# Kernel optimization log

Measured on AMD Instinct MI355X. Metric: run time of the kernel, lower is better.

The kernel has to match this reference:

```python
import jax, jax.numpy as jnp
import numpy as np

B = 1024        # batch of query guides
D = 768         # d_model
M = 50000       # memory bank size
K = 50          # k_neighbors
H = 8           # attention heads
HD = D // H     # head dim = 96
GH = 256        # gate hidden


def setup_inputs() -> dict:
    key = jax.random.key(0)
    ks = jax.random.split(key, 16)
    s = 0.02
    return {
        "query": jax.random.normal(ks[0], (B, D), jnp.float32),
        # memory bank buffers (initialized via initialize_memory in the original)
        "memory_keys": jax.random.normal(ks[1], (M, D), jnp.float32),
        "memory_values": jax.random.uniform(ks[2], (M, 1), jnp.float32, 0.5, 1.0),
        # MultiheadAttention in/out projections (batch_first, embed_dim=D, 8 heads)
        "Wq": jax.random.normal(ks[3], (D, D), jnp.float32) * s,
        "bq": jnp.zeros((D,), jnp.float32),
        "Wk": jax.random.normal(ks[4], (D, D), jnp.float32) * s,
        "bk": jnp.zeros((D,), jnp.float32),
        "Wv": jax.random.normal(ks[5], (D, D), jnp.float32) * s,
        "bv": jnp.zeros((D,), jnp.float32),
        "Wo": jax.random.normal(ks[6], (D, D), jnp.float32) * s,
        "bo": jnp.zeros((D,), jnp.float32),
        # gate MLP: Linear(2D, 256) -> ReLU -> Linear(256, 1) -> Sigmoid
        "Wg1": jax.random.normal(ks[7], (GH, 2 * D), jnp.float32) * s,
        "bg1": jnp.zeros((GH,), jnp.float32),
        "Wg2": jax.random.normal(ks[8], (1, GH), jnp.float32) * s,
        "bg2": jnp.zeros((1,), jnp.float32),
    }


def reference(query, memory_keys, memory_values,
              Wq, bq, Wk, bk, Wv, bv, Wo, bo, Wg1, bg1, Wg2, bg2):
    b = query.shape[0]
    # ---- retrieval: euclidean cdist + smallest-k ----
    q2 = jnp.sum(query * query, axis=-1, keepdims=True)      # (B,1)
    m2 = jnp.sum(memory_keys * memory_keys, axis=-1)          # (M,)
    d2 = q2 + m2[None, :] - 2.0 * (query @ memory_keys.T)     # (B,M)
    dists = jnp.sqrt(jnp.maximum(d2, 0.0))
    neg_top, idx = jax.lax.top_k(-dists, K)                   # smallest K
    distances = -neg_top                                      # (B,K)
    neighbor_keys = memory_keys[idx]                          # (B,K,D)
    neighbor_vals = memory_values[idx]                        # (B,K,1)

    # ---- cross-attention: 1 query token attending to K neighbors ----
    q = (query @ Wq.T + bq).reshape(b, H, HD)                 # (B,H,HD)
    kp = (neighbor_keys @ Wk.T + bk).reshape(b, K, H, HD)     # (B,K,H,HD)
    vp = (neighbor_keys @ Wv.T + bv).reshape(b, K, H, HD)
    scores = jnp.einsum('bhd,bkhd->bhk', q, kp) / jnp.sqrt(jnp.float32(HD))
    attn = jax.nn.softmax(scores, axis=-1)                    # (B,H,K)
    ctx = jnp.einsum('bhk,bkhd->bhd', attn, vp).reshape(b, D)
    context = ctx @ Wo.T + bo                                 # (B,D)

    similarity = jnp.exp(-distances / jnp.mean(distances))    # scalar mean over all
    weights = similarity / jnp.sum(similarity, axis=1, keepdims=True)
    rag_prediction = jnp.sum(neighbor_vals * weights[..., None], axis=1)  # (B,1)

    # ---- gated fusion ----
    combined = jnp.concatenate([query, context], axis=-1)     # (B,2D)
    hgate = jax.nn.relu(combined @ Wg1.T + bg1)
    gate_weight = jax.nn.sigmoid(hgate @ Wg2.T + bg2)         # (B,1)

    enhanced_embeddings = query + context                     # (B,D)
    return enhanced_embeddings, rag_prediction, gate_weight
```

## Files before the change

### kernel.cpp

```cpp
#include <hip/hip_runtime.h>

typedef unsigned int u32;
typedef unsigned short u16;
typedef unsigned char u8;
typedef signed char s8;
typedef unsigned long long u64;
typedef __bf16 bf16x8 __attribute__((ext_vector_type(8)));
typedef float f32x4 __attribute__((ext_vector_type(4)));
typedef int i32x4 __attribute__((ext_vector_type(4)));

#define DEVI __device__ __forceinline__

DEVI u16 f2bf(float x){ u32 u = __builtin_bit_cast(u32, x); return (u16)((u + 0x7fffu + ((u>>16)&1u)) >> 16); }
DEVI float bf2f(u16 h){ return __builtin_bit_cast(float, ((u32)h)<<16); }
DEVI u32 qz(float x){ int i = (int)rintf(x*25.4f); i = i>127?127:(i<-127?-127:i); return (u32)(u8)(s8)i; }

#define NB 1024
#define ND 768
#define NM 50000
#define NK 50
#define NH 8
#define CAP 2048
#define CAPX 256
#define S22 0.0031000062f
#define QINV 0.0393700787f

__global__ __launch_bounds__(256) void prep_all(const float* __restrict__ query, const float* __restrict__ mkeys,
    const float* __restrict__ Wq, const float* __restrict__ Wv, const float* __restrict__ Wo,
    const float* __restrict__ Wg1, const float* __restrict__ Wk,
    u16* __restrict__ qb, float* __restrict__ q2, s8* __restrict__ qi8, float* __restrict__ thr,
    s8* __restrict__ mi8, float* __restrict__ m2,
    u16* __restrict__ wqb, u16* __restrict__ wvb, u16* __restrict__ wob,
    u16* __restrict__ wg1b, u16* __restrict__ wkt)
{
  const int bid = blockIdx.x, t = threadIdx.x;
  if (bid < 12500){
    int r = bid*4 + (t>>6);
    int l = t & 63;
    const float4* s4 = (const float4*)(mkeys + (long)r*ND);
    u32* di = (u32*)(mi8 + (long)r*ND);
    float ss = 0.f;
    #pragma unroll
    for (int j=0;j<3;j++){
      float4 v = s4[l + j*64];
      ss += v.x*v.x + v.y*v.y + v.z*v.z + v.w*v.w;
      di[l+j*64] = qz(v.x) | (qz(v.y)<<8) | (qz(v.z)<<16) | (qz(v.w)<<24);
    }
    #pragma unroll
    for (int o=32;o;o>>=1) ss += __shfl_down(ss,o);
    if (l==0) m2[r]=ss;
  } else if (bid < 12756){
    int r = (bid-12500)*4 + (t>>6);
    int l = t & 63;
    const float4* s4 = (const float4*)(query + (long)r*ND);
    u32* dq = (u32*)(qb + (long)r*ND);
    u32* di = (u32*)(qi8 + (long)r*ND);
    float ss = 0.f;
    #pragma unroll
    for (int j=0;j<3;j++){
      float4 v = s4[l + j*64];
      ss += v.x*v.x + v.y*v.y + v.z*v.z + v.w*v.w;
      dq[(l+j*64)*2]   = ((u32)f2bf(v.y)<<16) | f2bf(v.x);
      dq[(l+j*64)*2+1] = ((u32)f2bf(v.w)<<16) | f2bf(v.z);
      di[l+j*64] = qz(v.x) | (qz(v.y)<<8) | (qz(v.z)<<16) | (qz(v.w)<<24);
    }
    #pragma unroll
    for (int o=32;o;o>>=1) ss += __shfl_down(ss,o);
    if (l==0){
      q2[r]=ss;
      thr[r] = ss + (float)ND - 2.5f*sqrtf(2.f*(float)ND + 4.f*ss);
    }
  } else {
    long i = (long)(bid-12756)*256 + t;
    const long NW = (long)ND*ND;
    if (i < NW){ wqb[i] = f2bf(Wq[i]); return; }
    i -= NW;
    if (i < NW){ wvb[i] = f2bf(Wv[i]); return; }
    i -= NW;
    if (i < NW){ wob[i] = f2bf(Wo[i]); return; }
    i -= NW;
    if (i < 256*2*ND){ wg1b[i] = f2bf(Wg1[i]); return; }
    i -= 256*2*ND;
    int h = (int)(i / (ND*96)); int rem = (int)(i % (ND*96)); int d = rem / 96; int hd = rem % 96;
    wkt[i] = f2bf(Wk[(long)(h*96+hd)*ND + d]);
  }
}

DEVI void i8_tile(u8* __restrict__ As, u8* __restrict__ Bs,
                  int m0, int n0, int cxcd,
                  const s8* __restrict__ A, int lda,
                  const s8* __restrict__ Bm, int ldb,
                  int Ndim, int Kbytes,
                  const float* __restrict__ q2, const float* __restrict__ m2, const float* __restrict__ thr,
                  float* __restrict__ cand_d2, int* __restrict__ cand_idx, int* __restrict__ cnt)
{
  const int t = threadIdx.x;
  const int lane = t & 63, w = t >> 6;
  i32x4 acc[2][8];
  #pragma unroll
  for (int m=0;m<2;m++)
    #pragma unroll
    for (int n=0;n<8;n++) acc[m][n] = i32x4{0,0,0,0};

  const int ra = t>>1, c0 = (t&1)*2;
  const int rb1 = ra+64;
  const int sw = (ra>>1)&3;
  const int s0 = ((c0  )^sw)*16, s1 = ((c0+1)^sw)*16;
  int jb0 = n0+ra;  if (jb0>=Ndim) jb0=Ndim-1;
  int jb1 = n0+rb1; if (jb1>=Ndim) jb1=Ndim-1;
  const s8* pa  = &A[(long)(m0+ra)*lda + c0*16];
  const s8* pb0 = &Bm[(long)jb0*ldb + c0*16];
  const s8* pb1 = &Bm[(long)jb1*ldb + c0*16];

  for (int k0=0; k0<Kbytes; k0+=64){
    __syncthreads();
    uint4 a0  = *(const uint4*)(pa  + k0);
    uint4 a1  = *(const uint4*)(pa  + k0 + 16);
    uint4 b00 = *(const uint4*)(pb0 + k0);
    uint4 b01 = *(const uint4*)(pb0 + k0 + 16);
    uint4 b10 = *(const uint4*)(pb1 + k0);
    uint4 b11 = *(const uint4*)(pb1 + k0 + 16);
    *(uint4*)&As[ra*64 + s0]  = a0;
    *(uint4*)&As[ra*64 + s1]  = a1;
    *(uint4*)&Bs[ra*64 + s0]  = b00;
    *(uint4*)&Bs[ra*64 + s1]  = b01;
    *(uint4*)&Bs[rb1*64 + s0] = b10;
    *(uint4*)&Bs[rb1*64 + s1] = b11;
    __syncthreads();
    i32x4 af[2], bfr[8];
    #pragma unroll
    for (int m=0;m<2;m++){
      int row = w*32 + m*16 + (lane&15);
      int slot = ((lane>>4) ^ ((row>>1)&3));
      af[m] = __builtin_bit_cast(i32x4, *(const uint4*)&As[row*64 + slot*16]);
    }
    #pragma unroll
    for (int n=0;n<8;n++){
      int row = n*16 + (lane&15);
      int slot = ((lane>>4) ^ ((row>>1)&3));
      bfr[n] = __builtin_bit_cast(i32x4, *(const uint4*)&Bs[row*64 + slot*16]);
    }
    #pragma unroll
    for (int m=0;m<2;m++)
      #pragma unroll
      for (int n=0;n<8;n++)
        acc[m][n] = __builtin_amdgcn_mfma_i32_16x16x64_i8(af[m], bfr[n], acc[m][n], 0,0,0);
  }

  const int g = lane>>4, li = lane&15;
  #pragma unroll
  for (int m=0;m<2;m++){
    #pragma unroll
    for (int q=0;q<4;q++){
      int r = m0 + w*32 + m*16 + (g<<2) + q;
      float qv = q2[r];
      float tv = thr[r];
      #pragma unroll
      for (int n=0;n<8;n++){
        int c = n0 + n*16 + li;
        int cc = c < Ndim ? c : 0;
        float v = S22 * (float)acc[m][n][q];
        float d2 = fmaxf(qv+m2[cc]-v, 0.f);
        bool hit = (c<Ndim) && (d2 <= tv);
        u64 mask = __ballot(hit);
        u32 bits = (u32)((mask >> (g*16)) & 0xffffull);
        int base = 0;
        if (li==0 && bits) base = atomicAdd(&cnt[cxcd*NB + r], (int)__popc(bits));
        base = __shfl(base, g*16);
        if (hit){
          int slot = base + (int)__popc(bits & ((1u<<li)-1u));
          if (slot < CAPX){
            cand_d2[(long)r*CAP + cxcd*CAPX + slot] = d2;
            cand_idx[(long)r*CAP + cxcd*CAPX + slot] = c;
          }
        }
      }
    }
  }
}

template<int FOUT>
DEVI void bf_tile(u16* __restrict__ As, u16* __restrict__ Bs,
                  int m0, int n0, int z,
                  const u16* __restrict__ A, int lda, long az,
                  const u16* __restrict__ Bm, int ldb, long bz,
                  int Ndim, int Kdim,
                  u16* __restrict__ Cb, float* __restrict__ Cf, int ldc, long cz,
                  const float* __restrict__ bias)
{
  A += (long)z*az; Bm += (long)z*bz;
  const int t = threadIdx.x;
  const int lane = t & 63, w = t >> 6;
  f32x4 acc[2][8];
  #pragma unroll
  for (int m=0;m<2;m++)
    #pragma unroll
    for (int n=0;n<8;n++) acc[m][n] = f32x4{0.f,0.f,0.f,0.f};

  const int ra = t>>1, c0 = (t&1)*2;
  const int rb1 = ra+64;
  const int sw = (ra>>1)&3;
  const int s0 = ((c0  )^sw)*8, s1 = ((c0+1)^sw)*8;
  int jb0 = n0+ra;  if (jb0>=Ndim) jb0=Ndim-1;
  int jb1 = n0+rb1; if (jb1>=Ndim) jb1=Ndim-1;
  const u16* pa  = &A[(long)(m0+ra)*lda + c0*8];
  const u16* pb0 = &Bm[(long)jb0*ldb + c0*8];
  const u16* pb1 = &Bm[(long)jb1*ldb + c0*8];

  for (int k0=0; k0<Kdim; k0+=32){
    __syncthreads();
    uint4 a0  = *(const uint4*)(pa  + k0);
    uint4 a1  = *(const uint4*)(pa  + k0 + 8);
    uint4 b00 = *(const uint4*)(pb0 + k0);
    uint4 b01 = *(const uint4*)(pb0 + k0 + 8);
    uint4 b10 = *(const uint4*)(pb1 + k0);
    uint4 b11 = *(const uint4*)(pb1 + k0 + 8);
    *(uint4*)&As[ra*32 + s0]  = a0;
    *(uint4*)&As[ra*32 + s1]  = a1;
    *(uint4*)&Bs[ra*32 + s0]  = b00;
    *(uint4*)&Bs[ra*32 + s1]  = b01;
    *(uint4*)&Bs[rb1*32 + s0] = b10;
    *(uint4*)&Bs[rb1*32 + s1] = b11;
    __syncthreads();
    bf16x8 af[2], bfr[8];
    #pragma unroll
    for (int m=0;m<2;m++){
      int row = w*32 + m*16 + (lane&15);
      int slot = ((lane>>4) ^ ((row>>1)&3));
      af[m] = __builtin_bit_cast(bf16x8, *(const uint4*)&As[row*32 + slot*8]);
    }
    #pragma unroll
    for (int n=0;n<8;n++){
      int row = n*16 + (lane&15);
      int slot = ((lane>>4) ^ ((row>>1)&3));
      bfr[n] = __builtin_bit_cast(bf16x8, *(const uint4*)&Bs[row*32 + slot*8]);
    }
    #pragma unroll
    for (int m=0;m<2;m++)
      #pragma unroll
      for (int n=0;n<8;n++)
        acc[m][n] = __builtin_amdgcn_mfma_f32_16x16x32_bf16(af[m], bfr[n], acc[m][n], 0,0,0);
  }

  #pragma unroll
  for (int m=0;m<2;m++){
    #pragma unroll
    for (int q=0;q<4;q++){
      int r = m0 + w*32 + m*16 + ((lane>>4)<<2) + q;
      #pragma unroll
      for (int n=0;n<8;n++){
        int c = n0 + n*16 + (lane&15);
        if (c >= Ndim) continue;
        float v = acc[m][n][q];
        if (bias) v += bias[c];
        if (FOUT==0) Cb[(long)r*ldc + (long)z*cz + c] = f2bf(v);
        else         Cf[(long)r*ldc + c] = v;
      }
    }
  }
}

__global__ __launch_bounds__(128)
void mega_a(const u16* __restrict__ qb, const u16* __restrict__ wqb,
            u16* __restrict__ qpb, const float* __restrict__ bq,
            const u16* __restrict__ wg1b, float* __restrict__ hg, const float* __restrict__ bg1)
{
  __shared__ u8 smem[12288];
  const int bid = blockIdx.x;
  if (bid < 96){
    int bx = bid & 15, by = bid >> 4;
    bf_tile<0>((u16*)smem, (u16*)(smem+4096), bx*64, by*128, 0,
               qb, ND, 0, wqb, ND, 0, ND, ND, qpb, nullptr, ND, 0, bq);
  } else {
    int b2 = bid - 96;
    int bx = b2 & 15, by = b2 >> 4;
    bf_tile<1>((u16*)smem, (u16*)(smem+4096), bx*64, by*128, 0,
               qb, ND, 0, wg1b, 2*ND, 0, 256, ND, nullptr, hg, 256, 0, bg1);
  }
}

__global__ __launch_bounds__(128)
void mega_b(const s8* __restrict__ qi8, const s8* __restrict__ mi8,
            const float* __restrict__ q2, const float* __restrict__ m2, const float* __restrict__ thr,
            float* __restrict__ cand_d2, int* __restrict__ cand_idx, int* __restrict__ cnt,
            const u16* __restrict__ qpb, const u16* __restrict__ wkt, u16* __restrict__ ubuf)
{
  __shared__ u8 smem[12288];
  const int bid = blockIdx.x;
  if (bid < 6272){
    int cxcd = bid & 7, j = bid >> 3;
    int xt = j & 15, yhi = j >> 4;
    int y = yhi*8 + cxcd;
    if (y >= 391) return;
    i8_tile(smem, smem+4096, xt*64, y*128, cxcd, qi8, ND, mi8, ND, NM, ND,
            q2, m2, thr, cand_d2, cand_idx, cnt);
  } else {
    int b2 = bid - 6272;
    int bx = b2 & 15, r = b2 >> 4;
    int by = r % 6, z = r / 6;
    bf_tile<0>((u16*)smem, (u16*)(smem+4096), bx*64, by*128, z,
               qpb, ND, 96, wkt, 96, (long)ND*96, ND, 96, ubuf, nullptr, NH*ND, ND, nullptr);
  }
}

template<int MODE>
__global__ __launch_bounds__(256)
void gemm_uni(const u16* __restrict__ A, int lda, long az,
              const u16* __restrict__ Bm, int ldb, long bz,
              int Ndim, int Kdim,
              float* __restrict__ Cf, u16* __restrict__ Cb, int ldc, long cz,
              const float* __restrict__ bias, long biasz,
              const float* __restrict__ qsrc, u16* __restrict__ out2, int ldo2)
{
  const int m0 = blockIdx.x*128, n0 = blockIdx.y*128, z = blockIdx.z;
  A += (long)z*az; Bm += (long)z*bz;

  const int t = threadIdx.x;
  const int lane = t & 63, wid = t >> 6;
  __shared__ u16 As[2][128*32], Bs[2][128*32];
  f32x4 acc[4][4];
  #pragma unroll
  for (int m=0;m<4;m++)
    #pragma unroll
    for (int n=0;n<4;n++) acc[m][n] = f32x4{0.f,0.f,0.f,0.f};

  const int wr = (wid>>1)*64, wc = (wid&1)*64;
  const int sr = t>>2, sc4 = t&3;
  const int r0 = sr, r1 = sr+64;
  const int sl0 = (sc4 ^ ((r0>>1)&3))*8, sl1 = (sc4 ^ ((r1>>1)&3))*8;
  int jb0 = n0+r0; if (jb0>=Ndim) jb0=Ndim-1;
  int jb1 = n0+r1; if (jb1>=Ndim) jb1=Ndim-1;
  const u16* pa0 = &A[(long)(m0+r0)*lda + sc4*8];
  const u16* pa1 = &A[(long)(m0+r1)*lda + sc4*8];
  const u16* pb0 = &Bm[(long)jb0*ldb + sc4*8];
  const u16* pb1 = &Bm[(long)jb1*ldb + sc4*8];

  uint4 pA0,pA1,pB0,pB1, qA0,qA1,qB0,qB1;
  #define LOADG(S, K0) { S##A0 = *(const uint4*)(pa0+(K0)); S##A1 = *(const uint4*)(pa1+(K0)); \
                         S##B0 = *(const uint4*)(pb0+(K0)); S##B1 = *(const uint4*)(pb1+(K0)); }
  #define STORELDS(BUF, S) { *(uint4*)&As[BUF][r0*32+sl0] = S##A0; *(uint4*)&As[BUF][r1*32+sl1] = S##A1; \
                             *(uint4*)&Bs[BUF][r0*32+sl0] = S##B0; *(uint4*)&Bs[BUF][r1*32+sl1] = S##B1; }

  auto compute = [&](const u16* __restrict__ Ab, const u16* __restrict__ Bb){
    bf16x8 af[4], bfr[4];
    #pragma unroll
    for (int m=0;m<4;m++){
      int row = wr + m*16 + (lane&15);
      int slot = ((lane>>4) ^ ((row>>1)&3));
      af[m] = __builtin_bit_cast(bf16x8, *(const uint4*)&Ab[row*32 + slot*8]);
    }
    #pragma unroll
    for (int n=0;n<4;n++){
      int row = wc + n*16 + (lane&15);
      int slot = ((lane>>4) ^ ((row>>1)&3));
      bfr[n] = __builtin_bit_cast(bf16x8, *(const uint4*)&Bb[row*32 + slot*8]);
    }
    #pragma unroll
    for (int m=0;m<4;m++)
      #pragma unroll
      for (int n=0;n<4;n++)
        acc[m][n] = __builtin_amdgcn_mfma_f32_16x16x32_bf16(af[m], bfr[n], acc[m][n], 0,0,0);
  };

  const int nt = Kdim >> 5;
  LOADG(p, 0);
  if (nt > 1) LOADG(q, 32);
  #pragma unroll 1
  for (int ti=0; ti<nt; ti+=2){
    STORELDS(0, p);
    asm volatile("s_waitcnt lgkmcnt(0)" ::: "memory");
    __builtin_amdgcn_s_barrier();
    if (ti+2 < nt) LOADG(p, (ti+2)*32);
    compute(As[0], Bs[0]);
    if (ti+1 < nt){
      STORELDS(1, q);
      asm volatile("s_waitcnt lgkmcnt(0)" ::: "memory");
      __builtin_amdgcn_s_barrier();
      if (ti+3 < nt) LOADG(q, (ti+3)*32);
      compute(As[1], Bs[1]);
    }
  }
  #undef LOADG
  #undef STORELDS

  const float* bz_p = bias ? bias + (long)z*biasz : nullptr;
  #pragma unroll
  for (int m=0;m<4;m++){
    #pragma unroll
    for (int n=0;n<4;n++){
      #pragma unroll
      for (int q=0;q<4;q++){
        int r = m0 + wr + m*16 + ((lane>>4)<<2) + q;
        int c = n0 + wc + n*16 + (lane&15);
        float v = acc[m][n][q];
        if (MODE==1){
          if (c<Ndim){ if(bz_p) v += bz_p[c]; Cb[(long)r*ldc + (long)z*cz + c] = f2bf(v); }
        } else if (MODE==5){
          if (c<Ndim){ Cf[(long)r*ldc + c] = fmaxf(Cf[(long)r*ldc + c] + v, 0.f); }
        } else {
          if (c<Ndim){
            float ctx = v + (bz_p?bz_p[c]:0.f);
            out2[(long)r*ldo2 + c] = f2bf(ctx);
            Cf[(long)r*ldc + c] = qsrc[(long)r*ND+c] + ctx;
          }
        }
      }
    }
  }
}

__global__ __launch_bounds__(256) void selattn(
    const float* __restrict__ cand_d2, const int* __restrict__ cand_idx, const int* __restrict__ cnt,
    const s8* __restrict__ mi8, const u16* __restrict__ ub,
    int* __restrict__ sel, float* __restrict__ dists, float* __restrict__ dsum,
    u16* __restrict__ sb)
{
  const int b = blockIdx.x, t = threadIdx.x;
  __shared__ u8 smemA[25*772*2];
  u64* arr = (u64*)smemA;
  u16* nkS = (u16*)smemA;
  __shared__ u16 uS[8*772];
  __shared__ float sc[NH*32];
  __shared__ float mh[NH], dh[NH], scS[NH];
  __shared__ int selS[NK];
  __shared__ float dS[NK];
  __shared__ int cS[8], oS[9];

  {
    const u32* src = (const u32*)&ub[(long)b*NH*ND];
    for (int i=t;i<NH*(ND/2);i+=256){
      int h = i/(ND/2), d = i%(ND/2);
      ((u32*)&uS[h*772])[d] = src[h*(ND/2)+d];
    }
  }
  if (t < 8){ int c = cnt[t*NB + b]; cS[t] = c > CAPX ? CAPX : c; }
  if (t >= 64 && t < 64+NH){ mh[t-64] = -1e30f; dh[t-64] = 0.f; }
  __syncthreads();
  if (t == 0){ oS[0]=0; for (int s=0;s<8;s++) oS[s+1]=oS[s]+cS[s]; }
  if (t < NK){ dS[t]=0.f; selS[t]=0; }
  __syncthreads();
  const int n = oS[8];
  for (int i=t;i<8*CAPX;i+=256){
    int s = i>>8, pos = i&(CAPX-1);
    if (pos < cS[s]){
      float d2 = fmaxf(cand_d2[(long)b*CAP + s*CAPX + pos],0.f);
      arr[oS[s]+pos] = ((u64)__builtin_bit_cast(u32, d2)<<32) | (u32)cand_idx[(long)b*CAP + s*CAPX + pos];
    }
  }
  __syncthreads();
  for (int i=t;i<n;i+=256){
    u64 me = arr[i];
    int rank = 0;
    for (int j=0;j<n;j++) rank += (arr[j] < me) ? 1 : 0;
    if (rank < NK){
      selS[rank] = (int)(u32)(me & 0xffffffffu);
      dS[rank] = sqrtf(__builtin_bit_cast(float, (u32)(me>>32)));
    }
  }
  __syncthreads();
  if (t < NK){ sel[b*NK+t] = selS[t]; dists[b*NK+t] = dS[t]; }
  if (t==0){ float s=0.f; for (int r=0;r<NK;r++) s+=dS[r]; dsum[b]=s; }
  __syncthreads();

  float sacc[3][NH];
  #pragma unroll
  for (int j=0;j<3;j++)
    #pragma unroll
    for (int h=0;h<NH;h++) sacc[j][h]=0.f;
  const float rs = 0.10206207261596575f;

  for (int half=0; half<2; ++half){
    if (half) __syncthreads();
    for (int k=0;k<25;k++){
      const u32* src = (const u32*)&mi8[(long)selS[half*25+k]*ND];
      if (t < 192){
        u32 a = src[t];
        float f0 = (float)(s8)(a & 0xff);
        float f1 = (float)(s8)((a>>8) & 0xff);
        float f2 = (float)(s8)((a>>16) & 0xff);
        float f3 = (float)(s8)(a>>24);
        u64 pk = (u64)f2bf(f0*QINV) | ((u64)f2bf(f1*QINV)<<16)
               | ((u64)f2bf(f2*QINV)<<32) | ((u64)f2bf(f3*QINV)<<48);
        *(u64*)&nkS[k*772 + t*4] = pk;
      }
    }
    __syncthreads();
    if (t < 200){
      const u32* nr = (const u32*)&nkS[(t%25)*772];
      const u32* ur = (const u32*)&uS[(t/25)*772];
      float acc = 0.f;
      #pragma unroll 8
      for (int d=0; d<ND/2; d++){
        u32 a = nr[d], uu = ur[d];
        acc += bf2f((u16)a)*bf2f((u16)uu) + bf2f((u16)(a>>16))*bf2f((u16)(uu>>16));
      }
      sc[(t/25)*32 + (t%25)] = acc*rs;
    }
    __syncthreads();
    if (t < NH){
      float mn = mh[t];
      #pragma unroll
      for (int k=0;k<25;k++) mn = fmaxf(mn, sc[t*32+k]);
      float scale = __expf(mh[t]-mn);
      float d = dh[t]*scale;
      #pragma unroll
      for (int k=0;k<25;k++){ float e = __expf(sc[t*32+k]-mn); sc[t*32+k]=e; d+=e; }
      mh[t]=mn; dh[t]=d; scS[t]=scale;
    }
    __syncthreads();
    #pragma unroll
    for (int j=0;j<3;j++){
      int dd = t + j*256;
      #pragma unroll
      for (int h=0;h<NH;h++) sacc[j][h] *= scS[h];
      for (int k=0;k<25;k++){
        float nv = bf2f(nkS[k*772+dd]);
        float w0,w1,w2,w3,w4,w5,w6,w7;
        w0=sc[0*32+k]; w1=sc[1*32+k]; w2=sc[2*32+k]; w3=sc[3*32+k];
        w4=sc[4*32+k]; w5=sc[5*32+k]; w6=sc[6*32+k]; w7=sc[7*32+k];
        sacc[j][0]+=w0*nv; sacc[j][1]+=w1*nv; sacc[j][2]+=w2*nv; sacc[j][3]+=w3*nv;
        sacc[j][4]+=w4*nv; sacc[j][5]+=w5*nv; sacc[j][6]+=w6*nv; sacc[j][7]+=w7*nv;
      }
    }
  }
  float inv[NH];
  #pragma unroll
  for (int h=0;h<NH;h++) inv[h] = 1.f/dh[h];
  #pragma unroll
  for (int j=0;j<3;j++){
    int dd = t + j*256;
    #pragma unroll
    for (int h=0;h<NH;h++) sb[(long)b*NH*ND + h*ND + dd] = f2bf(sacc[j][h]*inv[h]);
  }
}

__global__ void mean_kernel(const float* __restrict__ dsum, float* __restrict__ meanbuf){
  int t = threadIdx.x;
  float s=0.f; for (int i=t;i<NB;i+=256) s += dsum[i];
  __shared__ float red[256];
  red[t]=s; __syncthreads();
  #pragma unroll
  for (int st=128;st>0;st>>=1){ if(t<st) red[t]+=red[t+st]; __syncthreads(); }
  if (t==0){ float mean = red[0]/(float)(NB*NK); meanbuf[0]=mean; meanbuf[1]=1.f/mean; }
}

__global__ void final_k(const float* __restrict__ hg, const float* __restrict__ Wg2,
                        const float* __restrict__ bg2,
                        const int* __restrict__ sel, const float* __restrict__ dists,
                        const float* __restrict__ mvals, const float* __restrict__ meanbuf,
                        float* __restrict__ out_rag, float* __restrict__ out_gate){
  int b = blockIdx.x*4 + (threadIdx.x>>6);
  int l = threadIdx.x & 63;
  float s=0.f;
  for (int i=l;i<256;i+=64) s += hg[(long)b*256+i]*Wg2[i];
  float num=0.f, den=0.f;
  if (l < NK){
    float d = dists[b*NK+l];
    float v = mvals[sel[b*NK+l]];
    float e = __expf(-d*meanbuf[1]);
    num = e*v; den = e;
  }
  #pragma unroll
  for (int o=32;o;o>>=1){ s += __shfl_down(s,o); num += __shfl_down(num,o); den += __shfl_down(den,o); }
  if (l==0){
    out_gate[b] = 1.f/(1.f+__expf(-(s+bg2[0])));
    out_rag[b]  = num/den;
  }
}

extern "C" void kernel_launch(void* const* d_in, const int* in_sizes, int n_in,
                              void* d_out, int out_size, void* d_ws, size_t ws_size,
                              hipStream_t stream){
  const float* query = (const float*)d_in[0];
  const float* mkeys = (const float*)d_in[1];
  const float* mvals = (const float*)d_in[2];
  const float* Wq  = (const float*)d_in[3];
  const float* bq  = (const float*)d_in[4];
  const float* Wk  = (const float*)d_in[5];
  const float* Wv  = (const float*)d_in[7];
  const float* bv  = (const float*)d_in[8];
  const float* Wo  = (const float*)d_in[9];
  const float* bo  = (const float*)d_in[10];
  const float* Wg1 = (const float*)d_in[11];
  const float* bg1 = (const float*)d_in[12];
  const float* Wg2 = (const float*)d_in[13];
  const float* bg2 = (const float*)d_in[14];
  float* out = (float*)d_out;

  char* ws = (char*)d_ws;
  size_t off = 0;
  auto alloc = [&](size_t bytes)->char*{ char* p = ws + off; off += (bytes + 255) & ~(size_t)255; return p; };

  s8*    mi8   = (s8*)   alloc((size_t)NM*ND);
  s8*    qi8   = (s8*)   alloc((size_t)NB*ND);
  u16*   qb    = (u16*)  alloc((size_t)NB*ND*2);
  float* q2    = (float*)alloc(NB*4);
  float* m2    = (float*)alloc(NM*4);
  u16*   wqb   = (u16*)  alloc((size_t)ND*ND*2);
  u16*   wkt   = (u16*)  alloc((size_t)ND*ND*2);
  u16*   wvb   = (u16*)  alloc((size_t)ND*ND*2);
  u16*   wob   = (u16*)  alloc((size_t)ND*ND*2);
  u16*   wg1b  = (u16*)  alloc((size_t)256*2*ND*2);
  float* cand_d2 = (float*)alloc((size_t)NB*CAP*4);
  int*   cand_idx= (int*)  alloc((size_t)NB*CAP*4);
  float* thr   = (float*)alloc(NB*4);
  int*   cnt   = (int*)  alloc(8*NB*4);
  int*   sel   = (int*)  alloc((size_t)NB*NK*4);
  float* dists = (float*)alloc((size_t)NB*NK*4);
  float* dsum  = (float*)alloc(NB*4);
  float* meanbuf=(float*)alloc(256);
  u16*   qpb   = (u16*)  alloc((size_t)NB*ND*2);
  u16*   ubuf  = (u16*)  alloc((size_t)NB*NH*ND*2);
  u16*   sbuf  = (u16*)  alloc((size_t)NB*NH*ND*2);
  u16*   ctx2b = (u16*)  alloc((size_t)NB*ND*2);
  u16*   ctxb  = (u16*)  alloc((size_t)NB*ND*2);
  float* hg    = (float*)alloc((size_t)NB*256*4);
  (void)ws_size; (void)in_sizes; (void)n_in; (void)out_size;

  prep_all<<<23508, 256, 0, stream>>>(query, mkeys, Wq, Wv, Wo, Wg1, Wk,
      qb, q2, qi8, thr, mi8, m2, wqb, wvb, wob, wg1b, wkt);
  hipMemsetAsync(cnt, 0, 8*NB*sizeof(int), stream);

  mega_a<<<128, 128, 0, stream>>>(qb, wqb, qpb, bq, wg1b, hg, bg1);

  mega_b<<<7040, 128, 0, stream>>>(qi8, mi8, q2, m2, thr, cand_d2, cand_idx, cnt,
      qpb, wkt, ubuf);

  selattn<<<NB, 256, 0, stream>>>(cand_d2, cand_idx, cnt, mi8, ubuf, sel, dists, dsum, sbuf);
  mean_kernel<<<1, 256, 0, stream>>>(dsum, meanbuf);

  gemm_uni<1><<<dim3(NB/128, 1, NH), 256, 0, stream>>>(sbuf,NH*ND,ND, wvb,ND,(long)96*ND, 96,ND,
      nullptr,ctx2b,ND,96, bv,96, nullptr,nullptr,0);

  gemm_uni<4><<<dim3(NB/128, ND/128, 1), 256, 0, stream>>>(ctx2b,ND,0, wob,ND,0, ND,ND,
      out,nullptr,ND,0, bo,0, query, ctxb, ND);

  gemm_uni<5><<<dim3(NB/128, 2, 1), 256, 0, stream>>>(ctxb,ND,0, wg1b+ND,2*ND,0, 256,ND,
      hg,nullptr,256,0, nullptr,0, nullptr,nullptr,0);

  final_k<<<NB/4, 256, 0, stream>>>(hg, Wg2, bg2, sel, dists, mvals, meanbuf,
      out + (size_t)NB*ND, out + (size_t)NB*ND + NB);
}
```

Before: 445.1 us.

## Fold counter reset into prep, move gate GEMM into mega_b, shrink tail GEMM tiles

Zeroing of the candidate counters moves out of a separate memset and into extra blocks of the prep kernel, which saves one launch. The query-half gate GEMM moves from mega_a into mega_b as extra blocks, so it runs alongside the retrieval tiles. The three tail GEMMs change from 128x128 tiles with 256 threads and a double-buffered pipeline to 64x128 tiles with 128 threads and a single buffer. This gives more blocks on these small problems, at the cost of losing the load/compute overlap.

```diff
diff --git a/kernel.cpp b/kernel.cpp
--- a/kernel.cpp
+++ b/kernel.cpp
@@ -31,7 +31,7 @@
     u16* __restrict__ qb, float* __restrict__ q2, s8* __restrict__ qi8, float* __restrict__ thr,
     s8* __restrict__ mi8, float* __restrict__ m2,
     u16* __restrict__ wqb, u16* __restrict__ wvb, u16* __restrict__ wob,
-    u16* __restrict__ wg1b, u16* __restrict__ wkt)
+    u16* __restrict__ wg1b, u16* __restrict__ wkt, int* __restrict__ cnt)
 {
   const int bid = blockIdx.x, t = threadIdx.x;
   if (bid < 12500){
@@ -70,7 +70,7 @@
       q2[r]=ss;
       thr[r] = ss + (float)ND - 2.5f*sqrtf(2.f*(float)ND + 4.f*ss);
     }
-  } else {
+  } else if (bid < 23508){
     long i = (long)(bid-12756)*256 + t;
     const long NW = (long)ND*ND;
     if (i < NW){ wqb[i] = f2bf(Wq[i]); return; }
@@ -83,6 +83,9 @@
     i -= 256*2*ND;
     int h = (int)(i / (ND*96)); int rem = (int)(i % (ND*96)); int d = rem / 96; int hd = rem % 96;
     wkt[i] = f2bf(Wk[(long)(h*96+hd)*ND + d]);
+  } else {
+    int i = (bid-23508)*256 + t;
+    cnt[i] = 0; cnt[i+2048] = 0; cnt[i+4096] = 0; cnt[i+6144] = 0;
   }
 }
 
@@ -262,28 +265,22 @@
 
 __global__ __launch_bounds__(128)
 void mega_a(const u16* __restrict__ qb, const u16* __restrict__ wqb,
-            u16* __restrict__ qpb, const float* __restrict__ bq,
-            const u16* __restrict__ wg1b, float* __restrict__ hg, const float* __restrict__ bg1)
+            u16* __restrict__ qpb, const float* __restrict__ bq)
 {
   __shared__ u8 smem[12288];
   const int bid = blockIdx.x;
-  if (bid < 96){
-    int bx = bid & 15, by = bid >> 4;
-    bf_tile<0>((u16*)smem, (u16*)(smem+4096), bx*64, by*128, 0,
-               qb, ND, 0, wqb, ND, 0, ND, ND, qpb, nullptr, ND, 0, bq);
-  } else {
-    int b2 = bid - 96;
-    int bx = b2 & 15, by = b2 >> 4;
-    bf_tile<1>((u16*)smem, (u16*)(smem+4096), bx*64, by*128, 0,
-               qb, ND, 0, wg1b, 2*ND, 0, 256, ND, nullptr, hg, 256, 0, bg1);
-  }
+  int bx = bid & 15, by = bid >> 4;
+  bf_tile<0>((u16*)smem, (u16*)(smem+4096), bx*64, by*128, 0,
+             qb, ND, 0, wqb, ND, 0, ND, ND, qpb, nullptr, ND, 0, bq);
 }
 
 __global__ __launch_bounds__(128)
 void mega_b(const s8* __restrict__ qi8, const s8* __restrict__ mi8,
             const float* __restrict__ q2, const float* __restrict__ m2, const float* __restrict__ thr,
             float* __restrict__ cand_d2, int* __restrict__ cand_idx, int* __restrict__ cnt,
-            const u16* __restrict__ qpb, const u16* __restrict__ wkt, u16* __restrict__ ubuf)
+            const u16* __restrict__ qpb, const u16* __restrict__ wkt, u16* __restrict__ ubuf,
+            const u16* __restrict__ qb, const u16* __restrict__ wg1b,
+            float* __restrict__ hg, const float* __restrict__ bg1)
 {
   __shared__ u8 smem[12288];
   const int bid = blockIdx.x;
@@ -294,115 +291,104 @@
     if (y >= 391) return;
     i8_tile(smem, smem+4096, xt*64, y*128, cxcd, qi8, ND, mi8, ND, NM, ND,
             q2, m2, thr, cand_d2, cand_idx, cnt);
-  } else {
+  } else if (bid < 7040){
     int b2 = bid - 6272;
     int bx = b2 & 15, r = b2 >> 4;
     int by = r % 6, z = r / 6;
     bf_tile<0>((u16*)smem, (u16*)(smem+4096), bx*64, by*128, z,
                qpb, ND, 96, wkt, 96, (long)ND*96, ND, 96, ubuf, nullptr, NH*ND, ND, nullptr);
+  } else {
+    int b2 = bid - 7040;
+    int bx = b2 & 15, by = b2 >> 4;
+    bf_tile<1>((u16*)smem, (u16*)(smem+4096), bx*64, by*128, 0,
+               qb, ND, 0, wg1b, 2*ND, 0, 256, ND, nullptr, hg, 256, 0, bg1);
   }
 }
 
 template<int MODE>
-__global__ __launch_bounds__(256)
-void gemm_uni(const u16* __restrict__ A, int lda, long az,
+__global__ __launch_bounds__(128)
+void gemm64_t(const u16* __restrict__ A, int lda, long az,
               const u16* __restrict__ Bm, int ldb, long bz,
               int Ndim, int Kdim,
               float* __restrict__ Cf, u16* __restrict__ Cb, int ldc, long cz,
-              const float* __restrict__ bias, long biasz,
+              const float* __restrict__ bias,
               const float* __restrict__ qsrc, u16* __restrict__ out2, int ldo2)
 {
-  const int m0 = blockIdx.x*128, n0 = blockIdx.y*128, z = blockIdx.z;
+  const int m0 = blockIdx.x*64, n0 = blockIdx.y*128, z = blockIdx.z;
   A += (long)z*az; Bm += (long)z*bz;
-
+  __shared__ u16 As[64*32], Bs[128*32];
   const int t = threadIdx.x;
-  const int lane = t & 63, wid = t >> 6;
-  __shared__ u16 As[2][128*32], Bs[2][128*32];
-  f32x4 acc[4][4];
-  #pragma unroll
-  for (int m=0;m<4;m++)
-    #pragma unroll
-    for (int n=0;n<4;n++) acc[m][n] = f32x4{0.f,0.f,0.f,0.f};
-
-  const int wr = (wid>>1)*64, wc = (wid&1)*64;
-  const int sr = t>>2, sc4 = t&3;
-  const int r0 = sr, r1 = sr+64;
-  const int sl0 = (sc4 ^ ((r0>>1)&3))*8, sl1 = (sc4 ^ ((r1>>1)&3))*8;
-  int jb0 = n0+r0; if (jb0>=Ndim) jb0=Ndim-1;
-  int jb1 = n0+r1; if (jb1>=Ndim) jb1=Ndim-1;
-  const u16* pa0 = &A[(long)(m0+r0)*lda + sc4*8];
-  const u16* pa1 = &A[(long)(m0+r1)*lda + sc4*8];
-  const u16* pb0 = &Bm[(long)jb0*ldb + sc4*8];
-  const u16* pb1 = &Bm[(long)jb1*ldb + sc4*8];
-
-  uint4 pA0,pA1,pB0,pB1, qA0,qA1,qB0,qB1;
-  #define LOADG(S, K0) { S##A0 = *(const uint4*)(pa0+(K0)); S##A1 = *(const uint4*)(pa1+(K0)); \
-                         S##B0 = *(const uint4*)(pb0+(K0)); S##B1 = *(const uint4*)(pb1+(K0)); }
-  #define STORELDS(BUF, S) { *(uint4*)&As[BUF][r0*32+sl0] = S##A0; *(uint4*)&As[BUF][r1*32+sl1] = S##A1; \
-                             *(uint4*)&Bs[BUF][r0*32+sl0] = S##B0; *(uint4*)&Bs[BUF][r1*32+sl1] = S##B1; }
-
-  auto compute = [&](const u16* __restrict__ Ab, const u16* __restrict__ Bb){
-    bf16x8 af[4], bfr[4];
-    #pragma unroll
-    for (int m=0;m<4;m++){
-      int row = wr + m*16 + (lane&15);
+  const int lane = t & 63, w = t >> 6;
+  f32x4 acc[2][8];
+  #pragma unroll
+  for (int m=0;m<2;m++)
+    #pragma unroll
+    for (int n=0;n<8;n++) acc[m][n] = f32x4{0.f,0.f,0.f,0.f};
+
+  const int ra = t>>1, c0 = (t&1)*2;
+  const int rb1 = ra+64;
+  const int sw = (ra>>1)&3;
+  const int s0 = ((c0  )^sw)*8, s1 = ((c0+1)^sw)*8;
+  int jb0 = n0+ra;  if (jb0>=Ndim) jb0=Ndim-1;
+  int jb1 = n0+rb1; if (jb1>=Ndim) jb1=Ndim-1;
+  const u16* pa  = &A[(long)(m0+ra)*lda + c0*8];
+  const u16* pb0 = &Bm[(long)jb0*ldb + c0*8];
+  const u16* pb1 = &Bm[(long)jb1*ldb + c0*8];
+
+  for (int k0=0; k0<Kdim; k0+=32){
+    __syncthreads();
+    uint4 a0  = *(const uint4*)(pa  + k0);
+    uint4 a1  = *(const uint4*)(pa  + k0 + 8);
+    uint4 b00 = *(const uint4*)(pb0 + k0);
+    uint4 b01 = *(const uint4*)(pb0 + k0 + 8);
+    uint4 b10 = *(const uint4*)(pb1 + k0);
+    uint4 b11 = *(const uint4*)(pb1 + k0 + 8);
+    *(uint4*)&As[ra*32 + s0]  = a0;
+    *(uint4*)&As[ra*32 + s1]  = a1;
+    *(uint4*)&Bs[ra*32 + s0]  = b00;
+    *(uint4*)&Bs[ra*32 + s1]  = b01;
+    *(uint4*)&Bs[rb1*32 + s0] = b10;
+    *(uint4*)&Bs[rb1*32 + s1] = b11;
+    __syncthreads();
+    bf16x8 af[2], bfr[8];
+    #pragma unroll
+    for (int m=0;m<2;m++){
+      int row = w*32 + m*16 + (lane&15);
       int slot = ((lane>>4) ^ ((row>>1)&3));
-      af[m] = __builtin_bit_cast(bf16x8, *(const uint4*)&Ab[row*32 + slot*8]);
-    }
-    #pragma unroll
-    for (int n=0;n<4;n++){
-      int row = wc + n*16 + (lane&15);
+      af[m] = __builtin_bit_cast(bf16x8, *(const uint4*)&As[row*32 + slot*8]);
+    }
+    #pragma unroll
+    for (int n=0;n<8;n++){
+      int row = n*16 + (lane&15);
       int slot = ((lane>>4) ^ ((row>>1)&3));
-      bfr[n] = __builtin_bit_cast(bf16x8, *(const uint4*)&Bb[row*32 + slot*8]);
-    }
-    #pragma unroll
-    for (int m=0;m<4;m++)
-      #pragma unroll
-      for (int n=0;n<4;n++)
+      bfr[n] = __builtin_bit_cast(bf16x8, *(const uint4*)&Bs[row*32 + slot*8]);
+    }
+    #pragma unroll
+    for (int m=0;m<2;m++)
+      #pragma unroll
+      for (int n=0;n<8;n++)
         acc[m][n] = __builtin_amdgcn_mfma_f32_16x16x32_bf16(af[m], bfr[n], acc[m][n], 0,0,0);
-  };
-
-  const int nt = Kdim >> 5;
-  LOADG(p, 0);
-  if (nt > 1) LOADG(q, 32);
-  #pragma unroll 1
-  for (int ti=0; ti<nt; ti+=2){
-    STORELDS(0, p);
-    asm volatile("s_waitcnt lgkmcnt(0)" ::: "memory");
-    __builtin_amdgcn_s_barrier();
-    if (ti+2 < nt) LOADG(p, (ti+2)*32);
-    compute(As[0], Bs[0]);
-    if (ti+1 < nt){
-      STORELDS(1, q);
-      asm volatile("s_waitcnt lgkmcnt(0)" ::: "memory");
-      __builtin_amdgcn_s_barrier();
-      if (ti+3 < nt) LOADG(q, (ti+3)*32);
-      compute(As[1], Bs[1]);
-    }
-  }
-  #undef LOADG
-  #undef STORELDS
-
-  const float* bz_p = bias ? bias + (long)z*biasz : nullptr;
-  #pragma unroll
-  for (int m=0;m<4;m++){
-    #pragma unroll
-    for (int n=0;n<4;n++){
-      #pragma unroll
-      for (int q=0;q<4;q++){
-        int r = m0 + wr + m*16 + ((lane>>4)<<2) + q;
-        int c = n0 + wc + n*16 + (lane&15);
+  }
+
+  #pragma unroll
+  for (int m=0;m<2;m++){
+    #pragma unroll
+    for (int q=0;q<4;q++){
+      int r = m0 + w*32 + m*16 + ((lane>>4)<<2) + q;
+      #pragma unroll
+      for (int n=0;n<8;n++){
+        int c = n0 + n*16 + (lane&15);
+        if (c >= Ndim) continue;
         float v = acc[m][n][q];
         if (MODE==1){
-          if (c<Ndim){ if(bz_p) v += bz_p[c]; Cb[(long)r*ldc + (long)z*cz + c] = f2bf(v); }
+          if (bias) v += bias[c];
+          Cb[(long)r*ldc + (long)z*cz + c] = f2bf(v);
         } else if (MODE==5){
-          if (c<Ndim){ Cf[(long)r*ldc + c] = fmaxf(Cf[(long)r*ldc + c] + v, 0.f); }
+          Cf[(long)r*ldc + c] = fmaxf(Cf[(long)r*ldc + c] + v, 0.f);
         } else {
-          if (c<Ndim){
-            float ctx = v + (bz_p?bz_p[c]:0.f);
-            out2[(long)r*ldo2 + c] = f2bf(ctx);
-            Cf[(long)r*ldc + c] = qsrc[(long)r*ND+c] + ctx;
-          }
+          float ctx = v + (bias?bias[c]:0.f);
+          out2[(long)r*ldo2 + c] = f2bf(ctx);
+          Cf[(long)r*ldc + c] = qsrc[(long)r*ND+c] + ctx;
         }
       }
     }
@@ -617,26 +603,25 @@
   float* hg    = (float*)alloc((size_t)NB*256*4);
   (void)ws_size; (void)in_sizes; (void)n_in; (void)out_size;
 
-  prep_all<<<23508, 256, 0, stream>>>(query, mkeys, Wq, Wv, Wo, Wg1, Wk,
-      qb, q2, qi8, thr, mi8, m2, wqb, wvb, wob, wg1b, wkt);
-  hipMemsetAsync(cnt, 0, 8*NB*sizeof(int), stream);
-
-  mega_a<<<128, 128, 0, stream>>>(qb, wqb, qpb, bq, wg1b, hg, bg1);
-
-  mega_b<<<7040, 128, 0, stream>>>(qi8, mi8, q2, m2, thr, cand_d2, cand_idx, cnt,
-      qpb, wkt, ubuf);
+  prep_all<<<23516, 256, 0, stream>>>(query, mkeys, Wq, Wv, Wo, Wg1, Wk,
+      qb, q2, qi8, thr, mi8, m2, wqb, wvb, wob, wg1b, wkt, cnt);
+
+  mega_a<<<96, 128, 0, stream>>>(qb, wqb, qpb, bq);
+
+  mega_b<<<7072, 128, 0, stream>>>(qi8, mi8, q2, m2, thr, cand_d2, cand_idx, cnt,
+      qpb, wkt, ubuf, qb, wg1b, hg, bg1);
 
   selattn<<<NB, 256, 0, stream>>>(cand_d2, cand_idx, cnt, mi8, ubuf, sel, dists, dsum, sbuf);
   mean_kernel<<<1, 256, 0, stream>>>(dsum, meanbuf);
 
-  gemm_uni<1><<<dim3(NB/128, 1, NH), 256, 0, stream>>>(sbuf,NH*ND,ND, wvb,ND,(long)96*ND, 96,ND,
-      nullptr,ctx2b,ND,96, bv,96, nullptr,nullptr,0);
-
-  gemm_uni<4><<<dim3(NB/128, ND/128, 1), 256, 0, stream>>>(ctx2b,ND,0, wob,ND,0, ND,ND,
-      out,nullptr,ND,0, bo,0, query, ctxb, ND);
-
-  gemm_uni<5><<<dim3(NB/128, 2, 1), 256, 0, stream>>>(ctxb,ND,0, wg1b+ND,2*ND,0, 256,ND,
-      hg,nullptr,256,0, nullptr,0, nullptr,nullptr,0);
+  gemm64_t<1><<<dim3(16, 1, NH), 128, 0, stream>>>(sbuf,NH*ND,ND, wvb,ND,(long)96*ND, 96,ND,
+      nullptr,ctx2b,ND,96, bv, nullptr,nullptr,0);
+
+  gemm64_t<4><<<dim3(16, 6, 1), 128, 0, stream>>>(ctx2b,ND,0, wob,ND,0, ND,ND,
+      out,nullptr,ND,0, bo, query, ctxb, ND);
+
+  gemm64_t<5><<<dim3(16, 2, 1), 128, 0, stream>>>(ctxb,ND,0, wg1b+ND,2*ND,0, 256,ND,
+      hg,nullptr,256,0, nullptr, nullptr,nullptr,0);
 
   final_k<<<NB/4, 256, 0, stream>>>(hg, Wg2, bg2, sel, dists, mvals, meanbuf,
       out + (size_t)NB*ND, out + (size_t)NB*ND + NB);
```

After: 458.0 us. 2.9% more time.
